# Kernel tuning notes

Hardware: AMD Instinct MI355X
Metric: run time of the kernel (lower is better)

The kernel has to match this reference:

```python
import jax, jax.numpy as jnp
import numpy as np

NUM_SEGMENTS = 64  # batch_size, = batch_indices.max()+1 by construction


def setup_inputs() -> dict:
    key = jax.random.key(0)
    k1, k2 = jax.random.split(key)
    N, D = 1048576, 256
    features = jax.random.normal(k1, (N, D), dtype=jnp.float32)
    batch_indices = jnp.sort(jax.random.randint(k2, (N,), 0, NUM_SEGMENTS, dtype=jnp.int64))
    return {"features": features, "batch_indices": batch_indices}


def reference(features, batch_indices):
    # features: [N, D], batch_indices: [N] -> out: [B, 2*D]
    idx = batch_indices.astype(jnp.int32)
    counts = jax.ops.segment_sum(jnp.ones_like(features[:, 0]), idx,
                                 num_segments=NUM_SEGMENTS)  # [B]
    sums = jax.ops.segment_sum(features, idx, num_segments=NUM_SEGMENTS)  # [B, D]
    nonempty = counts > 0
    mean_feat = sums / jnp.maximum(counts, 1.0)[:, None]
    maxs = jax.ops.segment_max(features, idx, num_segments=NUM_SEGMENTS)  # [B, D]
    max_feat = jnp.where(nonempty[:, None], maxs, 0.0)
    mean_feat = jnp.where(nonempty[:, None], mean_feat, 0.0)
    return jnp.concatenate([mean_feat, max_feat], axis=1)  # [B, 2*D]
```

## Files before the change

kernel.cpp:

```cpp
#include <hip/hip_runtime.h>
#include <math.h>

#define D 256
#define SEGS 64
#define RPB 512
#define THREADS 256

typedef float f32x4 __attribute__((ext_vector_type(4)));

__device__ __forceinline__ unsigned enc_f32(float f) {
  unsigned u = __float_as_uint(f);
  return (u & 0x80000000u) ? ~u : (u | 0x80000000u);
}
__device__ __forceinline__ float dec_f32(unsigned k) {
  unsigned u = (k & 0x80000000u) ? (k ^ 0x80000000u) : ~k;
  return __uint_as_float(u);
}

__device__ __forceinline__ int idx_stride(const int* idx, int n) {
  return (idx[(size_t)n - 1] == 0) ? 2 : 1;
}

__global__ __launch_bounds__(THREADS, 8)
void agg_kernel(const float* __restrict__ feat, const int* __restrict__ idx,
                float* __restrict__ sums, unsigned* __restrict__ maxk,
                int* __restrict__ counts, int n) {
  __shared__ int s_idx[RPB];
  const int stride = idx_stride(idx, n);
  const int r0 = blockIdx.x * RPB;
  const int rows = min(RPB, n - r0);

  for (int i = threadIdx.x; i < rows; i += THREADS)
    s_idx[i] = idx[(size_t)(r0 + i) * stride];
  __syncthreads();

  const int lane = threadIdx.x & 63;
  const int wave = threadIdx.x >> 6;
  int i = wave * (RPB / 4);
  const int re = min(i + (RPB / 4), rows);
  if (i >= re) return;

  const float* base = feat + (size_t)r0 * D + lane * 4;
  const int last = s_idx[re - 1];

  while (i < re) {
    const int cur = s_idx[i];
    int j;
    if (cur == last) {
      j = re;
    } else {
      j = i + 1;
      while (s_idx[j] == cur) ++j;
    }

    f32x4 sum = {0.f, 0.f, 0.f, 0.f};
    f32x4 mx  = {-INFINITY, -INFINITY, -INFINITY, -INFINITY};
#pragma unroll 4
    for (int k = i; k < j; ++k) {
      const f32x4 v = __builtin_nontemporal_load(
          reinterpret_cast<const f32x4*>(base + (size_t)k * D));
      sum += v;
      mx.x = __builtin_fmaxf(mx.x, v.x);
      mx.y = __builtin_fmaxf(mx.y, v.y);
      mx.z = __builtin_fmaxf(mx.z, v.z);
      mx.w = __builtin_fmaxf(mx.w, v.w);
    }

    float* sp = sums + cur * D + lane * 4;
    atomicAdd(sp + 0, sum.x); atomicAdd(sp + 1, sum.y);
    atomicAdd(sp + 2, sum.z); atomicAdd(sp + 3, sum.w);
    unsigned* mp = maxk + cur * D + lane * 4;
    atomicMax(mp + 0, enc_f32(mx.x)); atomicMax(mp + 1, enc_f32(mx.y));
    atomicMax(mp + 2, enc_f32(mx.z)); atomicMax(mp + 3, enc_f32(mx.w));
    if (lane == 0) atomicAdd(&counts[cur], j - i);

    i = j;
  }
}

__global__ void finalize_kernel(const float* __restrict__ sums,
                                const unsigned* __restrict__ maxk,
                                const int* __restrict__ counts,
                                float* __restrict__ out) {
  int i = blockIdx.x * blockDim.x + threadIdx.x;
  if (i >= SEGS * 2 * D) return;
  int s = i / (2 * D);
  int j = i % (2 * D);
  int c = counts[s];
  float v;
  if (j < D)
    v = (c > 0) ? sums[s * D + j] / (float)c : 0.0f;
  else
    v = (c > 0) ? dec_f32(maxk[s * D + (j - D)]) : 0.0f;
  out[i] = v;
}

extern "C" void kernel_launch(void* const* d_in, const int* in_sizes, int n_in,
                              void* d_out, int out_size, void* d_ws, size_t ws_size,
                              hipStream_t stream) {
  const float* feat = (const float*)d_in[0];
  const int*   idx  = (const int*)d_in[1];
  const int n = in_sizes[1];
  float* out = (float*)d_out;

  char* ws = (char*)d_ws;
  float*    sums   = (float*)ws;
  unsigned* maxk   = (unsigned*)(ws + SEGS * D * 4);
  int*      counts = (int*)(ws + 2 * SEGS * D * 4);

  const size_t zero_bytes = 2 * (size_t)SEGS * D * 4 + SEGS * 4;
  hipMemsetAsync(ws, 0, zero_bytes, stream);

  const int nblocks = (n + RPB - 1) / RPB;
  agg_kernel<<<nblocks, THREADS, 0, stream>>>(feat, idx, sums, maxk, counts, n);

  finalize_kernel<<<(SEGS * 2 * D + 255) / 256, 256, 0, stream>>>(
      sums, maxk, counts, out);
}
```

Before: 217.8 us.

## Precompute segment boundaries via binary search and drop per-block index staging

Adds an init kernel that zeroes the accumulators and binary-searches the sorted index array to find each segment's end offset, replacing the memset and the counts atomics. The aggregation kernel no longer stages indices in shared memory. Each wave finds its current segment with a ballot over the boundaries held one per lane and steps through segments with shuffles. Counts are derived from boundary differences in finalize. Unroll is raised to 8 and launch bounds relaxed, so the change trades the per-block index loads and syncthreads for one small extra kernel launch doing serial binary searches.

```diff
diff --git a/kernel.cpp b/kernel.cpp
--- a/kernel.cpp
+++ b/kernel.cpp
@@ -17,45 +17,49 @@
   return __uint_as_float(u);
 }
 
-__device__ __forceinline__ int idx_stride(const int* idx, int n) {
-  return (idx[(size_t)n - 1] == 0) ? 2 : 1;
+__global__ void init_kernel(const int* __restrict__ idx, int n,
+                            float* __restrict__ sums,
+                            unsigned* __restrict__ maxk,
+                            int* __restrict__ bounds) {
+  const int s = blockIdx.x;
+  if (threadIdx.x < D) {
+    sums[s * D + threadIdx.x] = 0.0f;
+    maxk[s * D + threadIdx.x] = 0u;
+  }
+  if (threadIdx.x == 0) {
+    const int stride = (idx[(size_t)n - 1] == 0) ? 2 : 1;
+    const int v = s + 1;
+    int lo = 0, hi = n;
+    while (lo < hi) {
+      int mid = (lo + hi) >> 1;
+      if (idx[(size_t)mid * stride] < v) lo = mid + 1; else hi = mid;
+    }
+    bounds[s + 1] = lo;
+    if (s == 0) bounds[0] = 0;
+  }
 }
 
-__global__ __launch_bounds__(THREADS, 8)
-void agg_kernel(const float* __restrict__ feat, const int* __restrict__ idx,
-                float* __restrict__ sums, unsigned* __restrict__ maxk,
-                int* __restrict__ counts, int n) {
-  __shared__ int s_idx[RPB];
-  const int stride = idx_stride(idx, n);
-  const int r0 = blockIdx.x * RPB;
-  const int rows = min(RPB, n - r0);
-
-  for (int i = threadIdx.x; i < rows; i += THREADS)
-    s_idx[i] = idx[(size_t)(r0 + i) * stride];
-  __syncthreads();
-
+__global__ __launch_bounds__(THREADS, 4)
+void agg_kernel(const float* __restrict__ feat, const int* __restrict__ bounds,
+                float* __restrict__ sums, unsigned* __restrict__ maxk, int n) {
   const int lane = threadIdx.x & 63;
   const int wave = threadIdx.x >> 6;
-  int i = wave * (RPB / 4);
-  const int re = min(i + (RPB / 4), rows);
+  int i = blockIdx.x * RPB + wave * (RPB / 4);
+  const int re = min(i + (RPB / 4), n);
   if (i >= re) return;
 
-  const float* base = feat + (size_t)r0 * D + lane * 4;
-  const int last = s_idx[re - 1];
+  const int b_end = bounds[lane + 1];
+  int cur = (int)__popcll(__ballot(b_end <= i));
 
-  while (i < re) {
-    const int cur = s_idx[i];
-    int j;
-    if (cur == last) {
-      j = re;
-    } else {
-      j = i + 1;
-      while (s_idx[j] == cur) ++j;
-    }
+  const float* base = feat + lane * 4;
+
+  while (true) {
+    const int e = __shfl(b_end, cur);
+    const int j = min(re, e);
 
     f32x4 sum = {0.f, 0.f, 0.f, 0.f};
     f32x4 mx  = {-INFINITY, -INFINITY, -INFINITY, -INFINITY};
-#pragma unroll 4
+#pragma unroll 8
     for (int k = i; k < j; ++k) {
       const f32x4 v = __builtin_nontemporal_load(
           reinterpret_cast<const f32x4*>(base + (size_t)k * D));
@@ -72,27 +76,28 @@
     unsigned* mp = maxk + cur * D + lane * 4;
     atomicMax(mp + 0, enc_f32(mx.x)); atomicMax(mp + 1, enc_f32(mx.y));
     atomicMax(mp + 2, enc_f32(mx.z)); atomicMax(mp + 3, enc_f32(mx.w));
-    if (lane == 0) atomicAdd(&counts[cur], j - i);
 
+    if (j >= re) break;
     i = j;
+    do { ++cur; } while (__shfl(b_end, cur) <= i);
   }
 }
 
 __global__ void finalize_kernel(const float* __restrict__ sums,
                                 const unsigned* __restrict__ maxk,
-                                const int* __restrict__ counts,
+                                const int* __restrict__ bounds,
                                 float* __restrict__ out) {
-  int i = blockIdx.x * blockDim.x + threadIdx.x;
-  if (i >= SEGS * 2 * D) return;
-  int s = i / (2 * D);
-  int j = i % (2 * D);
-  int c = counts[s];
+  int t = blockIdx.x * blockDim.x + threadIdx.x;
+  if (t >= SEGS * 2 * D) return;
+  int s = t / (2 * D);
+  int j = t % (2 * D);
+  int c = bounds[s + 1] - bounds[s];
   float v;
   if (j < D)
     v = (c > 0) ? sums[s * D + j] / (float)c : 0.0f;
   else
     v = (c > 0) ? dec_f32(maxk[s * D + (j - D)]) : 0.0f;
-  out[i] = v;
+  out[t] = v;
 }
 
 extern "C" void kernel_launch(void* const* d_in, const int* in_sizes, int n_in,
@@ -106,14 +111,13 @@
   char* ws = (char*)d_ws;
   float*    sums   = (float*)ws;
   unsigned* maxk   = (unsigned*)(ws + SEGS * D * 4);
-  int*      counts = (int*)(ws + 2 * SEGS * D * 4);
+  int*      bounds = (int*)(ws + 2 * SEGS * D * 4);
 
-  const size_t zero_bytes = 2 * (size_t)SEGS * D * 4 + SEGS * 4;
-  hipMemsetAsync(ws, 0, zero_bytes, stream);
+  init_kernel<<<SEGS, THREADS, 0, stream>>>(idx, n, sums, maxk, bounds);
 
   const int nblocks = (n + RPB - 1) / RPB;
-  agg_kernel<<<nblocks, THREADS, 0, stream>>>(feat, idx, sums, maxk, counts, n);
+  agg_kernel<<<nblocks, THREADS, 0, stream>>>(feat, bounds, sums, maxk, n);
 
-  finalize_kernel<<<(SEGS * 2 * D + 255) / 256, 256, 0, stream>>>(
-      sums, maxk, counts, out);
+  finalize_kernel<<<(SEGS * 2 * D + THREADS - 1) / THREADS, THREADS, 0, stream>>>(
+      sums, maxk, bounds, out);
 }
```

Result: no change. 217.8 us, median of 2 (-0.0%).
